# Optimization experiments

Measured on AMD Instinct MI355X. Metric: run time of the kernel, lower is better.

The kernel has to match this reference:

```python
import jax, jax.numpy as jnp
import numpy as np

B, N, V, H, R, A, IN, K = 64, 512, 64, 512, 4, 18, 128, 32
EPS = 1e-8


def setup_inputs() -> dict:
    key = jax.random.key(0)
    ks = jax.random.split(key, 20)
    g = lambda i, shape, s=1.0: jax.random.normal(ks[i], shape, jnp.float32) * s
    u = lambda i, shape: jax.random.uniform(ks[i], shape, dtype=jnp.float32)
    cin = IN + R * V
    return dict(
        x=g(0, (B, IN)),
        h=g(1, (B, H), 0.1),
        c=g(2, (B, H), 0.1),
        memory=g(3, (B, N, V), 0.1),
        read_weights=u(4, (B, R, N)),
        write_weights=u(5, (B, N)),
        usage=u(6, (B, N)),
        link_matrix=u(7, (B, N, N)) * 0.01,
        precedence_weights=u(8, (B, N)),
        W_ih=g(9, (4 * H, cin), 0.05), W_hh=g(10, (4 * H, H), 0.05),
        b_ih=jnp.zeros(4 * H, jnp.float32), b_hh=jnp.zeros(4 * H, jnp.float32),
        W_read=g(11, (R, V + 4, H), 0.05), b_read=jnp.zeros((R, V + 4), jnp.float32),
        W_write=g(12, (3 * V + 3, H), 0.05), b_write=jnp.zeros(3 * V + 3, jnp.float32),
        W_pol=g(13, (A, H), 0.05), b_pol=jnp.zeros(A, jnp.float32),
        W_val=g(14, (1, H), 0.05), b_val=jnp.zeros(1, jnp.float32),
    )


def reference(x, h, c, memory, read_weights, write_weights, usage, link_matrix,
              precedence_weights, W_ih, W_hh, b_ih, b_hh, W_read, b_read,
              W_write, b_write, W_pol, b_pol, W_val, b_val):
    # ---- read heads (vectorized over R) ----
    ro = jnp.einsum('roh,bh->bro', W_read, h) + b_read            # [B,R,V+4]
    rkey = ro[..., :V]
    rbeta = jax.nn.softplus(ro[..., V])                           # [B,R]
    rpi = jax.nn.softmax(ro[..., V + 1:V + 4], axis=-1)           # backward/content/forward gates
    mem_norm = jnp.maximum(jnp.linalg.norm(memory, axis=-1), EPS)  # [B,N]
    key_norm = jnp.maximum(jnp.linalg.norm(rkey, axis=-1), EPS)    # [B,R]
    sim = jnp.einsum('bnv,brv->brn', memory, rkey) / (mem_norm[:, None, :] * key_norm[..., None])
    scores = rbeta[..., None] * sim                                # [B,R,N]
    kth = jax.lax.top_k(scores, K)[0][..., -1:]                    # sparse top-k mask
    cw = jax.nn.softmax(jnp.where(scores >= kth, scores, -jnp.inf), axis=-1)
    fw = jnp.einsum('bnm,brm->brn', link_matrix, read_weights)     # forward weighting L w
    bw = jnp.einsum('bmn,brm->brn', link_matrix, read_weights)     # backward weighting L^T w
    w_r = rpi[..., 0:1] * bw + rpi[..., 1:2] * cw + rpi[..., 2:3] * fw  # [B,R,N]
    rvec = jnp.einsum('brn,bnv->brv', w_r, memory).reshape(B, R * V)
    # ---- LSTM controller (torch LSTMCell gate order i,f,g,o) ----
    gates = jnp.concatenate([x, rvec], -1) @ W_ih.T + h @ W_hh.T + b_ih + b_hh
    i_g, f_g, g_g, o_g = jnp.split(gates, 4, axis=-1)
    c_new = jax.nn.sigmoid(f_g) * c + jax.nn.sigmoid(i_g) * jnp.tanh(g_g)
    h_new = jax.nn.sigmoid(o_g) * jnp.tanh(c_new)
    # ---- write head ----
    wo = h_new @ W_write.T + b_write                               # [B,3V+3]
    wkey = wo[:, :V]
    erase = jax.nn.sigmoid(wo[:, V:2 * V])
    add = jnp.tanh(wo[:, 2 * V:3 * V])
    wbeta = jax.nn.softplus(wo[:, 3 * V])
    g_a = jax.nn.sigmoid(wo[:, 3 * V + 1])
    g_w = jax.nn.sigmoid(wo[:, 3 * V + 2])
    wkey_norm = jnp.maximum(jnp.linalg.norm(wkey, axis=-1), EPS)
    wsim = jnp.einsum('bnv,bv->bn', memory, wkey) / (mem_norm * wkey_norm[:, None])
    cw_w = jax.nn.softmax(wbeta[:, None] * wsim, axis=-1)
    # allocation weighting from sorted usage (DNC Eq. 1)
    idx = jnp.argsort(usage, axis=-1)
    u_sorted = jnp.take_along_axis(usage, idx, -1)
    prod_prev = jnp.concatenate([jnp.ones((B, 1), usage.dtype), jnp.cumprod(u_sorted, -1)[:, :-1]], -1)
    a_sorted = (1.0 - u_sorted) * prod_prev
    alloc = jnp.take_along_axis(a_sorted, jnp.argsort(idx, -1), -1)
    write_w = g_w[:, None] * (g_a[:, None] * alloc + (1.0 - g_a)[:, None] * cw_w)  # [B,N]
    # ---- memory erase/add ----
    mem_new = memory * (1.0 - write_w[:, :, None] * erase[:, None, :]) + write_w[:, :, None] * add[:, None, :]
    # ---- usage (psi detached as in torch.no_grad) ----
    psi = jax.lax.stop_gradient(jnp.prod(1.0 - w_r, axis=1))
    usage_new = (usage + write_weights - usage * write_weights) * psi
    # ---- link matrix + precedence ----
    ws = jnp.sum(write_w, -1, keepdims=True)
    prec_new = (1.0 - ws) * precedence_weights + write_w
    decay = (1.0 - write_w[:, :, None]) * (1.0 - write_w[:, None, :])
    link_new = decay * link_matrix + write_w[:, :, None] * precedence_weights[:, None, :]
    link_new = link_new * (1.0 - jnp.eye(N, dtype=link_new.dtype))
    # ---- actor/critic heads ----
    logits = h_new @ W_pol.T + b_pol
    value = h_new @ W_val.T + b_val
    return (logits, value, h_new, c_new, mem_new, w_r, write_w, usage_new, link_new, prec_new)
```

## Files before the change

### kernel.cpp

```cpp
#include <hip/hip_runtime.h>
#include <math.h>

constexpr int Bb = 64, Nn = 512, Vv = 64, Hh = 512, Rr = 4, Aa = 18, INp = 128, KTOP = 32;
constexpr int CIN = 384;
constexpr int WOUT = 195;
#define EPSf 1e-8f

__device__ __forceinline__ float sigmoidf(float x){ return 1.f/(1.f+expf(-x)); }
__device__ __forceinline__ float softplusf(float x){ return (x>20.f)? x : log1pf(expf(x)); }
__device__ __forceinline__ float wave_reduce(float v){
  #pragma unroll
  for(int o=32;o>0;o>>=1) v += __shfl_down(v, o, 64);
  return v;
}

__global__ void k_read_proj(const float* __restrict__ Wr, const float* __restrict__ br,
                            const float* __restrict__ h, float* __restrict__ ro) {
  int bid = blockIdx.x;
  int b = bid / 68;
  int p = (bid % 68) * 4 + (threadIdx.x >> 6);
  int lane = threadIdx.x & 63;
  const float* wrow = Wr + p * Hh;
  const float* hb = h + b * Hh;
  float acc = 0.f;
  #pragma unroll
  for (int t = 0; t < 8; ++t) { int k = lane + 64*t; acc += wrow[k] * hb[k]; }
  acc = wave_reduce(acc);
  if (lane == 0) ro[b*272 + p] = acc + br[p];
}

__global__ void k_scores(const float* __restrict__ mem, const float* __restrict__ ro,
                         float* __restrict__ scores) {
  int row = blockIdx.x*4 + (threadIdx.x>>6);
  int lane = threadIdx.x & 63;
  int b = row >> 9, n = row & 511;
  float m = mem[row*Vv + lane];
  float mn = wave_reduce(m*m);
  #pragma unroll
  for (int r = 0; r < Rr; ++r) {
    const float* rob = ro + b*272 + r*68;
    float kv = rob[lane];
    float s  = wave_reduce(m*kv);
    float k2 = wave_reduce(kv*kv);
    if (lane == 0) {
      float rbeta = softplusf(rob[64]);
      float mnc = fmaxf(sqrtf(mn), EPSf);
      float knc = fmaxf(sqrtf(k2), EPSf);
      scores[(b*Rr + r)*Nn + n] = rbeta * s / (mnc * knc);
    }
  }
}

__global__ void k_topk_cw(const float* __restrict__ scores, float* __restrict__ cw) {
  __shared__ float sv[512];
  __shared__ float so[512];
  __shared__ float red[256];
  int br = blockIdx.x;
  int tid = threadIdx.x;
  const float* srow = scores + br*Nn;
  for (int i = tid; i < 512; i += 256) { float v = srow[i]; sv[i]=v; so[i]=v; }
  __syncthreads();
  for (int k = 2; k <= 512; k <<= 1) {
    for (int j = k>>1; j > 0; j >>= 1) {
      for (int i = tid; i < 512; i += 256) {
        int ixj = i ^ j;
        if (ixj > i) {
          float a = sv[i], c = sv[ixj];
          bool descSeg = ((i & k) == 0);
          bool sw = descSeg ? (a < c) : (a > c);
          if (sw) { sv[i]=c; sv[ixj]=a; }
        }
      }
      __syncthreads();
    }
  }
  float kth = sv[KTOP-1];
  float mx = sv[0];
  float lsum = 0.f;
  for (int i = tid; i < 512; i += 256) {
    float v = so[i];
    lsum += (v >= kth) ? expf(v - mx) : 0.f;
  }
  red[tid] = lsum; __syncthreads();
  for (int s2 = 128; s2 > 0; s2 >>= 1) {
    if (tid < s2) red[tid] += red[tid+s2];
    __syncthreads();
  }
  float inv = 1.f / red[0];
  for (int i = tid; i < 512; i += 256) {
    float v = so[i];
    cw[br*Nn + i] = (v >= kth) ? expf(v - mx)*inv : 0.f;
  }
}

__global__ void k_fwbw(const float* __restrict__ link, const float* __restrict__ rw,
                       float* __restrict__ fw, float* __restrict__ bwpart) {
  __shared__ float bl[4][4][512];
  int b  = blockIdx.x >> 3;
  int ch = blockIdx.x & 7;
  int wv = threadIdx.x >> 6, lane = threadIdx.x & 63;
  const float* rwb = rw + b*Rr*Nn;
  float rwv[4][8];
  #pragma unroll
  for (int r = 0; r < 4; ++r)
    #pragma unroll
    for (int t = 0; t < 8; ++t) rwv[r][t] = rwb[r*512 + lane + 64*t];
  float bwacc[8][4] = {};
  const float* lb = link + (size_t)b*Nn*Nn;
  int n0 = ch*64 + wv*16;
  for (int i = 0; i < 16; ++i) {
    int n = n0 + i;
    float lk[8];
    #pragma unroll
    for (int t = 0; t < 8; ++t) lk[t] = lb[n*512 + lane + 64*t];
    float s0 = rwb[n], s1 = rwb[512+n], s2 = rwb[1024+n], s3 = rwb[1536+n];
    float f0=0,f1=0,f2=0,f3=0;
    #pragma unroll
    for (int t = 0; t < 8; ++t) {
      float lv = lk[t];
      f0 += lv*rwv[0][t]; f1 += lv*rwv[1][t]; f2 += lv*rwv[2][t]; f3 += lv*rwv[3][t];
      bwacc[t][0] += lv*s0; bwacc[t][1] += lv*s1; bwacc[t][2] += lv*s2; bwacc[t][3] += lv*s3;
    }
    f0 = wave_reduce(f0); f1 = wave_reduce(f1);
    f2 = wave_reduce(f2); f3 = wave_reduce(f3);
    if (lane == 0) {
      fw[(b*Rr+0)*Nn+n] = f0; fw[(b*Rr+1)*Nn+n] = f1;
      fw[(b*Rr+2)*Nn+n] = f2; fw[(b*Rr+3)*Nn+n] = f3;
    }
  }
  #pragma unroll
  for (int t = 0; t < 8; ++t)
    #pragma unroll
    for (int r = 0; r < 4; ++r) bl[wv][r][lane + 64*t] = bwacc[t][r];
  __syncthreads();
  int tid = threadIdx.x;
  #pragma unroll
  for (int q = 0; q < 8; ++q) {
    int idx = q*256 + tid;
    int r = idx >> 9, j = idx & 511;
    float v = bl[0][r][j] + bl[1][r][j] + bl[2][r][j] + bl[3][r][j];
    bwpart[((size_t)(ch*Bb + b)*Rr + r)*Nn + j] = v;
  }
}

__global__ void k_wr_usage(const float* __restrict__ bwpart, const float* __restrict__ cw,
                           const float* __restrict__ fw, const float* __restrict__ ro,
                           const float* __restrict__ usage, const float* __restrict__ wwt,
                           float* __restrict__ out_wr, float* __restrict__ out_usage,
                           float* __restrict__ ws_rvec) {
  int idx = blockIdx.x*256 + threadIdx.x;
  if (idx < Bb*Rr*Vv) ws_rvec[idx] = 0.f;
  int b = idx >> 9, n = idx & 511;
  float psi = 1.f;
  #pragma unroll
  for (int r = 0; r < Rr; ++r) {
    int br = b*Rr + r;
    const float* rob = ro + b*272 + r*68;
    float e0 = rob[65], e1 = rob[66], e2 = rob[67];
    float m = fmaxf(e0, fmaxf(e1, e2));
    float x0 = expf(e0-m), x1 = expf(e1-m), x2 = expf(e2-m);
    float inv = 1.f/(x0+x1+x2);
    float bwv = 0.f;
    #pragma unroll
    for (int chh = 0; chh < 8; ++chh)
      bwv += bwpart[((size_t)(chh*Bb + b)*Rr + r)*Nn + n];
    float w = (x0*bwv + x1*cw[br*Nn+n] + x2*fw[br*Nn+n]) * inv;
    out_wr[br*Nn+n] = w;
    psi *= (1.f - w);
  }
  float u = usage[idx], wt = wwt[idx];
  out_usage[idx] = (u + wt - u*wt) * psi;
}

__global__ void k_rvec(const float* __restrict__ wr, const float* __restrict__ mem,
                       float* __restrict__ rvec) {
  int b = blockIdx.x >> 3;
  int ch = blockIdx.x & 7;
  int r = threadIdx.x >> 6, v = threadIdx.x & 63;
  const float* wrow = wr + (b*Rr + r)*Nn;
  const float* mb = mem + (size_t)b*Nn*Vv;
  float acc = 0.f;
  #pragma unroll 4
  for (int t = 0; t < 64; ++t) {
    int n = ch*64 + t;
    acc += wrow[n] * mb[n*Vv + v];
  }
  atomicAdd(&rvec[(b*Rr+r)*Vv + v], acc);
}

__global__ void k_gates(const float* __restrict__ x, const float* __restrict__ rvec,
                        const float* __restrict__ h, const float* __restrict__ Wih,
                        const float* __restrict__ Whh, const float* __restrict__ bih,
                        const float* __restrict__ bhh, float* __restrict__ gates) {
  int gid = blockIdx.x*4 + (threadIdx.x>>6);
  int lane = threadIdx.x & 63;
  int jt = gid >> 4;
  int bt = gid & 15;
  float acc[4][4] = {};
  #pragma unroll
  for (int t = 0; t < 6; ++t) {
    int k = lane + 64*t;
    float u[4], w[4];
    #pragma unroll
    for (int i = 0; i < 4; ++i) {
      int b = bt*4 + i;
      u[i] = (k < INp) ? x[b*INp + k] : rvec[b*(Rr*Vv) + k - INp];
      w[i] = Wih[(jt*4+i)*CIN + k];
    }
    #pragma unroll
    for (int jj = 0; jj < 4; ++jj)
      #pragma unroll
      for (int bb = 0; bb < 4; ++bb) acc[jj][bb] += w[jj]*u[bb];
  }
  #pragma unroll
  for (int t = 0; t < 8; ++t) {
    int k = lane + 64*t;
    float u[4], w[4];
    #pragma unroll
    for (int i = 0; i < 4; ++i) {
      u[i] = h[(bt*4+i)*Hh + k];
      w[i] = Whh[(jt*4+i)*Hh + k];
    }
    #pragma unroll
    for (int jj = 0; jj < 4; ++jj)
      #pragma unroll
      for (int bb = 0; bb < 4; ++bb) acc[jj][bb] += w[jj]*u[bb];
  }
  #pragma unroll
  for (int jj = 0; jj < 4; ++jj)
    #pragma unroll
    for (int bb = 0; bb < 4; ++bb) {
      float v = wave_reduce(acc[jj][bb]);
      if (lane == 0) {
        int j = jt*4 + jj, b = bt*4 + bb;
        gates[b*(4*Hh) + j] = v + bih[j] + bhh[j];
      }
    }
}

__global__ void k_lstm(const float* __restrict__ gates, const float* __restrict__ c,
                       float* __restrict__ out_h, float* __restrict__ out_c) {
  int idx = blockIdx.x*256 + threadIdx.x;
  int b = idx >> 9, hh = idx & 511;
  const float* g = gates + b*2048;
  float ig = sigmoidf(g[hh]), fg = sigmoidf(g[512+hh]);
  float gg = tanhf(g[1024+hh]), og = sigmoidf(g[1536+hh]);
  float cn = fg * c[idx] + ig * gg;
  float hn = og * tanhf(cn);
  out_c[idx] = cn; out_h[idx] = hn;
}

__global__ void k_wopol(const float* __restrict__ hn, const float* __restrict__ Ww,
                        const float* __restrict__ bw_, const float* __restrict__ Wp,
                        const float* __restrict__ bp, const float* __restrict__ Wv,
                        const float* __restrict__ bv, float* __restrict__ wo,
                        float* __restrict__ out_logits, float* __restrict__ out_value) {
  int gid = blockIdx.x*4 + (threadIdx.x>>6);
  int lane = threadIdx.x & 63;
  int b = gid / 214, o = gid % 214;
  const float* wrow;
  if (o < WOUT) wrow = Ww + o*Hh;
  else if (o < WOUT + Aa) wrow = Wp + (o-WOUT)*Hh;
  else wrow = Wv;
  const float* hb = hn + b*Hh;
  float acc = 0.f;
  #pragma unroll
  for (int t = 0; t < 8; ++t) { int k = lane+64*t; acc += hb[k]*wrow[k]; }
  acc = wave_reduce(acc);
  if (lane == 0) {
    if (o < WOUT) wo[b*WOUT+o] = acc + bw_[o];
    else if (o < WOUT + Aa) out_logits[b*Aa + (o-WOUT)] = acc + bp[o-WOUT];
    else out_value[b] = acc + bv[0];
  }
}

__global__ void k_wsim(const float* __restrict__ mem, const float* __restrict__ wo,
                       float* __restrict__ wsim) {
  int row = blockIdx.x*4 + (threadIdx.x>>6);
  int lane = threadIdx.x & 63;
  int b = row >> 9;
  const float* wob = wo + b*WOUT;
  float kv = wob[lane];
  float m = mem[row*Vv + lane];
  float s  = wave_reduce(m*kv);
  float mn = wave_reduce(m*m);
  float k2 = wave_reduce(kv*kv);
  if (lane == 0) {
    float wbeta = softplusf(wob[192]);
    wsim[row] = wbeta * s / (fmaxf(sqrtf(mn),EPSf) * fmaxf(sqrtf(k2),EPSf));
  }
}

__global__ void k_alloc(const float* __restrict__ usage, const float* __restrict__ wo,
                        const float* __restrict__ wsim, const float* __restrict__ prec,
                        float* __restrict__ out_ww, float* __restrict__ out_prec) {
  __shared__ float uv[512];
  __shared__ int   ui[512];
  __shared__ float cp[512];
  __shared__ float al[512];
  __shared__ float red[256];
  int b = blockIdx.x, tid = threadIdx.x;
  float s0 = wsim[b*Nn + tid], s1 = wsim[b*Nn + tid + 256];
  red[tid] = fmaxf(s0, s1); __syncthreads();
  for (int s2=128; s2>0; s2>>=1){ if (tid<s2) red[tid]=fmaxf(red[tid],red[tid+s2]); __syncthreads(); }
  float mx = red[0]; __syncthreads();
  float e0 = expf(s0-mx), e1 = expf(s1-mx);
  red[tid] = e0+e1; __syncthreads();
  for (int s2=128; s2>0; s2>>=1){ if (tid<s2) red[tid]+=red[tid+s2]; __syncthreads(); }
  float cinv = 1.f/red[0];
  float c0 = e0*cinv, c1 = e1*cinv;
  __syncthreads();
  for (int i = tid; i < 512; i += 256) { uv[i] = usage[b*Nn+i]; ui[i] = i; }
  __syncthreads();
  for (int k = 2; k <= 512; k <<= 1) {
    for (int j = k>>1; j > 0; j >>= 1) {
      for (int i = tid; i < 512; i += 256) {
        int ixj = i ^ j;
        if (ixj > i) {
          float av = uv[i], bv = uv[ixj];
          int ai = ui[i], bi = ui[ixj];
          bool gt = (av > bv) || (av == bv && ai > bi);
          bool asc = ((i & k) == 0);
          bool sw = asc ? gt : !gt;
          if (sw) { uv[i]=bv; uv[ixj]=av; ui[i]=bi; ui[ixj]=ai; }
        }
      }
      __syncthreads();
    }
  }
  for (int i = tid; i < 512; i += 256) cp[i] = uv[i];
  __syncthreads();
  for (int d = 1; d < 512; d <<= 1) {
    float t0 = cp[tid]     * ((tid >= d)     ? cp[tid-d]     : 1.f);
    float t1 = cp[tid+256] * ((tid+256 >= d) ? cp[tid+256-d] : 1.f);
    __syncthreads();
    cp[tid] = t0; cp[tid+256] = t1;
    __syncthreads();
  }
  for (int i = tid; i < 512; i += 256) {
    float pp = (i == 0) ? 1.f : cp[i-1];
    al[ui[i]] = (1.f - uv[i]) * pp;
  }
  __syncthreads();
  float ga = sigmoidf(wo[b*WOUT+193]);
  float gw = sigmoidf(wo[b*WOUT+194]);
  int n0 = tid, n1 = tid+256;
  float wv0 = gw * (ga*al[n0] + (1.f-ga)*c0);
  float wv1 = gw * (ga*al[n1] + (1.f-ga)*c1);
  out_ww[b*Nn+n0] = wv0; out_ww[b*Nn+n1] = wv1;
  red[tid] = wv0 + wv1; __syncthreads();
  for (int s2=128; s2>0; s2>>=1){ if (tid<s2) red[tid]+=red[tid+s2]; __syncthreads(); }
  float wsum = red[0];
  out_prec[b*Nn+n0] = (1.f - wsum)*prec[b*Nn+n0] + wv0;
  out_prec[b*Nn+n1] = (1.f - wsum)*prec[b*Nn+n1] + wv1;
}

__global__ void k_memlink(const float* __restrict__ link, const float* __restrict__ ww,
                          const float* __restrict__ prec, const float* __restrict__ mem,
                          const float* __restrict__ wo, float* __restrict__ out_link,
                          float* __restrict__ out_mem) {
  int bid = blockIdx.x;
  if (bid < 16384) {
    int idx4 = bid*256 + threadIdx.x;
    int base = idx4*4;
    int b = base >> 18;
    int rem = base & 262143;
    int i = rem >> 9;
    int j0 = rem & 511;
    float wi = ww[b*Nn + i];
    float fi = 1.f - wi;
    float4 lv = *(const float4*)(link + base);
    float4 wj = *(const float4*)(ww + b*Nn + j0);
    float4 pj = *(const float4*)(prec + b*Nn + j0);
    float4 o;
    o.x = fi*(1.f-wj.x)*lv.x + wi*pj.x;
    o.y = fi*(1.f-wj.y)*lv.y + wi*pj.y;
    o.z = fi*(1.f-wj.z)*lv.z + wi*pj.z;
    o.w = fi*(1.f-wj.w)*lv.w + wi*pj.w;
    if (i >= j0 && i < j0+4) {
      if (i == j0) o.x = 0.f;
      else if (i == j0+1) o.y = 0.f;
      else if (i == j0+2) o.z = 0.f;
      else o.w = 0.f;
    }
    *(float4*)(out_link + base) = o;
  } else {
    int idx4 = (bid - 16384)*256 + threadIdx.x;
    int base = idx4*4;
    int b = base >> 15;
    int rem = base & 32767;
    int n = rem >> 6;
    int v0 = rem & 63;
    float w = ww[b*Nn + n];
    const float* wob = wo + b*WOUT;
    float4 m = *(const float4*)(mem + base);
    float4 o;
    float e, a;
    e = sigmoidf(wob[64+v0+0]); a = tanhf(wob[128+v0+0]); o.x = m.x*(1.f-w*e)+w*a;
    e = sigmoidf(wob[64+v0+1]); a = tanhf(wob[128+v0+1]); o.y = m.y*(1.f-w*e)+w*a;
    e = sigmoidf(wob[64+v0+2]); a = tanhf(wob[128+v0+2]); o.z = m.z*(1.f-w*e)+w*a;
    e = sigmoidf(wob[64+v0+3]); a = tanhf(wob[128+v0+3]); o.w = m.w*(1.f-w*e)+w*a;
    *(float4*)(out_mem + base) = o;
  }
}

extern "C" void kernel_launch(void* const* d_in, const int* in_sizes, int n_in,
                              void* d_out, int out_size, void* d_ws, size_t ws_size,
                              hipStream_t stream) {
  const float* x    = (const float*)d_in[0];
  const float* h    = (const float*)d_in[1];
  const float* c    = (const float*)d_in[2];
  const float* mem  = (const float*)d_in[3];
  const float* rw   = (const float*)d_in[4];
  const float* wwt  = (const float*)d_in[5];
  const float* usage= (const float*)d_in[6];
  const float* link = (const float*)d_in[7];
  const float* prec = (const float*)d_in[8];
  const float* Wih  = (const float*)d_in[9];
  const float* Whh  = (const float*)d_in[10];
  const float* bih  = (const float*)d_in[11];
  const float* bhh  = (const float*)d_in[12];
  const float* Wr   = (const float*)d_in[13];
  const float* br   = (const float*)d_in[14];
  const float* Ww   = (const float*)d_in[15];
  const float* bw_  = (const float*)d_in[16];
  const float* Wp   = (const float*)d_in[17];
  const float* bp   = (const float*)d_in[18];
  const float* Wv   = (const float*)d_in[19];
  const float* bv   = (const float*)d_in[20];

  float* out = (float*)d_out;
  float* o_logits = out + 0;
  float* o_value  = out + 1152;
  float* o_h      = out + 1216;
  float* o_c      = out + 33984;
  float* o_mem    = out + 66752;
  float* o_wr     = out + 2163904;
  float* o_ww     = out + 2294976;
  float* o_usage  = out + 2327744;
  float* o_link   = out + 2360512;
  float* o_prec   = out + 19137728;

  float* ws = (float*)d_ws;
  float* ws_ro     = ws;
  float* ws_sc     = ws + 17408;
  float* ws_cw     = ws + 148480;
  float* ws_fw     = ws + 279552;
  float* ws_bwpart = ws + 410624;
  float* ws_rvec   = ws + 1459200;
  float* ws_gates  = ws + 1475584;
  float* ws_wo     = ws + 1606656;
  float* ws_wsim   = ws + 1619136;

  k_read_proj <<<dim3(Bb*68),        dim3(256), 0, stream>>>(Wr, br, h, ws_ro);
  k_scores    <<<dim3(Bb*Nn/4),      dim3(256), 0, stream>>>(mem, ws_ro, ws_sc);
  k_topk_cw   <<<dim3(Bb*Rr),        dim3(256), 0, stream>>>(ws_sc, ws_cw);
  k_fwbw      <<<dim3(Bb*8),         dim3(256), 0, stream>>>(link, rw, ws_fw, ws_bwpart);
  k_wr_usage  <<<dim3(Bb*Nn/256),    dim3(256), 0, stream>>>(ws_bwpart, ws_cw, ws_fw, ws_ro, usage, wwt, o_wr, o_usage, ws_rvec);
  k_rvec      <<<dim3(Bb*8),         dim3(256), 0, stream>>>(o_wr, mem, ws_rvec);
  k_gates     <<<dim3(2048),         dim3(256), 0, stream>>>(x, ws_rvec, h, Wih, Whh, bih, bhh, ws_gates);
  k_lstm      <<<dim3(Bb*Hh/256),    dim3(256), 0, stream>>>(ws_gates, c, o_h, o_c);
  k_wopol     <<<dim3(Bb*214/4),     dim3(256), 0, stream>>>(o_h, Ww, bw_, Wp, bp, Wv, bv, ws_wo, o_logits, o_value);
  k_wsim      <<<dim3(Bb*Nn/4),      dim3(256), 0, stream>>>(mem, ws_wo, ws_wsim);
  k_alloc     <<<dim3(Bb),           dim3(256), 0, stream>>>(usage, ws_wo, ws_wsim, prec, o_ww, o_prec);
  k_memlink   <<<dim3(16384+2048),   dim3(256), 0, stream>>>(link, o_ww, prec, mem, ws_wo, o_link, o_mem);
}
```

Before: 347.6 us.

## Fuse kernels, replace bitonic sorts with rank counting, precompute read-head params

Merges the read projection with the forward/backward link pass in one launch, folds the read-vector product into the read-weight kernel, and fuses the LSTM gate GEMV with the cell update. The bitonic sorts in top-k and allocation become O(N^2) rank counting on packed order keys. Softmax gates, key norms and inverse memory norms are computed once and reused. Launch count, sync barriers and intermediate traffic drop. The cost is fewer blocks in the read-vector kernel (128) and serial 512-step rank loops per thread.

```diff
diff --git a/kernel.cpp b/kernel.cpp
--- a/kernel.cpp
+++ b/kernel.cpp
@@ -13,188 +13,209 @@
   for(int o=32;o>0;o>>=1) v += __shfl_down(v, o, 64);
   return v;
 }
-
-__global__ void k_read_proj(const float* __restrict__ Wr, const float* __restrict__ br,
-                            const float* __restrict__ h, float* __restrict__ ro) {
-  int bid = blockIdx.x;
-  int b = bid / 68;
-  int p = (bid % 68) * 4 + (threadIdx.x >> 6);
-  int lane = threadIdx.x & 63;
-  const float* wrow = Wr + p * Hh;
-  const float* hb = h + b * Hh;
-  float acc = 0.f;
-  #pragma unroll
-  for (int t = 0; t < 8; ++t) { int k = lane + 64*t; acc += wrow[k] * hb[k]; }
-  acc = wave_reduce(acc);
-  if (lane == 0) ro[b*272 + p] = acc + br[p];
+__device__ __forceinline__ unsigned f2ord(float f){
+  unsigned u = __float_as_uint(f);
+  return (u & 0x80000000u) ? ~u : (u | 0x80000000u);
+}
+
+__global__ void k_stage1(const float* __restrict__ link, const float* __restrict__ rw,
+                         const float* __restrict__ Wr, const float* __restrict__ brd,
+                         const float* __restrict__ h,
+                         float* __restrict__ fw, float* __restrict__ bwpart,
+                         float* __restrict__ rvec,
+                         float* __restrict__ ro, float* __restrict__ rp) {
+  __shared__ float bl[4][4][512];
+  __shared__ float sh[512];
+  __shared__ float sro[68];
+  if (blockIdx.x < 512) {
+    if (blockIdx.x < 64) rvec[blockIdx.x*256 + threadIdx.x] = 0.f;
+    int b  = blockIdx.x >> 3;
+    int ch = blockIdx.x & 7;
+    int wv = threadIdx.x >> 6, lane = threadIdx.x & 63;
+    const float* rwb = rw + b*Rr*Nn;
+    float rwv[4][8];
+    #pragma unroll
+    for (int r = 0; r < 4; ++r)
+      #pragma unroll
+      for (int t = 0; t < 8; ++t) rwv[r][t] = rwb[r*512 + lane + 64*t];
+    float bwacc[8][4] = {};
+    const float* lb = link + (size_t)b*Nn*Nn;
+    int n0 = ch*64 + wv*16;
+    for (int i = 0; i < 16; ++i) {
+      int n = n0 + i;
+      float lk[8];
+      #pragma unroll
+      for (int t = 0; t < 8; ++t) lk[t] = lb[n*512 + lane + 64*t];
+      float s0 = rwb[n], s1 = rwb[512+n], s2 = rwb[1024+n], s3 = rwb[1536+n];
+      float f0=0,f1=0,f2=0,f3=0;
+      #pragma unroll
+      for (int t = 0; t < 8; ++t) {
+        float lv = lk[t];
+        f0 += lv*rwv[0][t]; f1 += lv*rwv[1][t]; f2 += lv*rwv[2][t]; f3 += lv*rwv[3][t];
+        bwacc[t][0] += lv*s0; bwacc[t][1] += lv*s1; bwacc[t][2] += lv*s2; bwacc[t][3] += lv*s3;
+      }
+      f0 = wave_reduce(f0); f1 = wave_reduce(f1);
+      f2 = wave_reduce(f2); f3 = wave_reduce(f3);
+      if (lane == 0) {
+        fw[(b*Rr+0)*Nn+n] = f0; fw[(b*Rr+1)*Nn+n] = f1;
+        fw[(b*Rr+2)*Nn+n] = f2; fw[(b*Rr+3)*Nn+n] = f3;
+      }
+    }
+    #pragma unroll
+    for (int t = 0; t < 8; ++t)
+      #pragma unroll
+      for (int r = 0; r < 4; ++r) bl[wv][r][lane + 64*t] = bwacc[t][r];
+    __syncthreads();
+    int tid = threadIdx.x;
+    #pragma unroll
+    for (int q = 0; q < 8; ++q) {
+      int idx = q*256 + tid;
+      int r = idx >> 9, j = idx & 511;
+      float v = bl[0][r][j] + bl[1][r][j] + bl[2][r][j] + bl[3][r][j];
+      bwpart[((size_t)(ch*Bb + b)*Rr + r)*Nn + j] = v;
+    }
+  } else {
+    int blk = blockIdx.x - 512;
+    int b = blk >> 2, r = blk & 3;
+    int wv = threadIdx.x >> 6, lane = threadIdx.x & 63;
+    const float* hb = h + b*Hh;
+    for (int i = threadIdx.x; i < 512; i += 256) sh[i] = hb[i];
+    __syncthreads();
+    const float* wbase = Wr + (size_t)(r*68)*Hh;
+    for (int q = 0; q < 17; ++q) {
+      int p = wv*17 + q;
+      const float* wrow = wbase + (size_t)p*Hh;
+      float acc = 0.f;
+      #pragma unroll
+      for (int t = 0; t < 8; ++t) { int k = lane + 64*t; acc += wrow[k]*sh[k]; }
+      acc = wave_reduce(acc);
+      if (lane == 0) sro[p] = acc + brd[r*68 + p];
+    }
+    __syncthreads();
+    if (threadIdx.x < 68) ro[b*272 + r*68 + threadIdx.x] = sro[threadIdx.x];
+    if (wv == 0) {
+      float kv = sro[lane];
+      float k2 = wave_reduce(kv*kv);
+      if (lane == 0) {
+        float rbeta = softplusf(sro[64]);
+        float sc = rbeta / fmaxf(sqrtf(k2), EPSf);
+        float e0 = sro[65], e1 = sro[66], e2 = sro[67];
+        float mm = fmaxf(e0, fmaxf(e1, e2));
+        float x0 = expf(e0-mm), x1 = expf(e1-mm), x2 = expf(e2-mm);
+        float inv = 1.f/(x0+x1+x2);
+        float* rpb = rp + (b*4 + r)*4;
+        rpb[0] = sc; rpb[1] = x0*inv; rpb[2] = x1*inv; rpb[3] = x2*inv;
+      }
+    }
+  }
 }
 
 __global__ void k_scores(const float* __restrict__ mem, const float* __restrict__ ro,
-                         float* __restrict__ scores) {
+                         const float* __restrict__ rp, float* __restrict__ scores,
+                         float* __restrict__ invmn) {
   int row = blockIdx.x*4 + (threadIdx.x>>6);
   int lane = threadIdx.x & 63;
   int b = row >> 9, n = row & 511;
   float m = mem[row*Vv + lane];
-  float mn = wave_reduce(m*m);
-  #pragma unroll
-  for (int r = 0; r < Rr; ++r) {
-    const float* rob = ro + b*272 + r*68;
-    float kv = rob[lane];
-    float s  = wave_reduce(m*kv);
-    float k2 = wave_reduce(kv*kv);
-    if (lane == 0) {
-      float rbeta = softplusf(rob[64]);
-      float mnc = fmaxf(sqrtf(mn), EPSf);
-      float knc = fmaxf(sqrtf(k2), EPSf);
-      scores[(b*Rr + r)*Nn + n] = rbeta * s / (mnc * knc);
-    }
+  const float* rob = ro + b*272;
+  float v0 = m*m;
+  float v1 = m * rob[lane];
+  float v2 = m * rob[68  + lane];
+  float v3 = m * rob[136 + lane];
+  float v4 = m * rob[204 + lane];
+  #pragma unroll
+  for (int o = 32; o > 0; o >>= 1) {
+    v0 += __shfl_down(v0,o,64); v1 += __shfl_down(v1,o,64);
+    v2 += __shfl_down(v2,o,64); v3 += __shfl_down(v3,o,64);
+    v4 += __shfl_down(v4,o,64);
+  }
+  if (lane == 0) {
+    float im = 1.f / fmaxf(sqrtf(v0), EPSf);
+    invmn[row] = im;
+    const float* rpb = rp + b*16;
+    scores[(b*4+0)*Nn+n] = rpb[0]  * v1 * im;
+    scores[(b*4+1)*Nn+n] = rpb[4]  * v2 * im;
+    scores[(b*4+2)*Nn+n] = rpb[8]  * v3 * im;
+    scores[(b*4+3)*Nn+n] = rpb[12] * v4 * im;
   }
 }
 
 __global__ void k_topk_cw(const float* __restrict__ scores, float* __restrict__ cw) {
-  __shared__ float sv[512];
-  __shared__ float so[512];
-  __shared__ float red[256];
-  int br = blockIdx.x;
+  __shared__ unsigned long long sk[512];
+  __shared__ float sred[4];
+  __shared__ float skv[2];
+  int br = blockIdx.x, tid = threadIdx.x;
+  float v0 = scores[br*Nn + tid], v1 = scores[br*Nn + tid + 256];
+  unsigned long long k0 = ((unsigned long long)f2ord(v0) << 32) | (unsigned)(511 - tid);
+  unsigned long long k1 = ((unsigned long long)f2ord(v1) << 32) | (unsigned)(255 - tid);
+  sk[tid] = k0; sk[tid+256] = k1;
+  __syncthreads();
+  int c0 = 0, c1 = 0;
+  #pragma unroll 8
+  for (int j = 0; j < 512; ++j) {
+    unsigned long long kj = sk[j];
+    c0 += (kj > k0); c1 += (kj > k1);
+  }
+  if (c0 == KTOP-1) skv[0] = v0;
+  if (c1 == KTOP-1) skv[0] = v1;
+  if (c0 == 0) skv[1] = v0;
+  if (c1 == 0) skv[1] = v1;
+  __syncthreads();
+  float kth = skv[0], mx = skv[1];
+  float e0 = (v0 >= kth) ? expf(v0-mx) : 0.f;
+  float e1 = (v1 >= kth) ? expf(v1-mx) : 0.f;
+  float s = wave_reduce(e0+e1);
+  if ((tid&63) == 0) sred[tid>>6] = s;
+  __syncthreads();
+  float inv = 1.f/(sred[0]+sred[1]+sred[2]+sred[3]);
+  cw[br*Nn+tid]     = e0*inv;
+  cw[br*Nn+tid+256] = e1*inv;
+}
+
+__global__ void k_wrrv(const float* __restrict__ bwpart, const float* __restrict__ cw,
+                       const float* __restrict__ fw, const float* __restrict__ rp,
+                       const float* __restrict__ usage, const float* __restrict__ wwt,
+                       const float* __restrict__ mem,
+                       float* __restrict__ out_wr, float* __restrict__ out_usage,
+                       float* __restrict__ rvec) {
+  __shared__ float swr[4][256];
+  int b = blockIdx.x >> 1, ch = blockIdx.x & 1;
   int tid = threadIdx.x;
-  const float* srow = scores + br*Nn;
-  for (int i = tid; i < 512; i += 256) { float v = srow[i]; sv[i]=v; so[i]=v; }
-  __syncthreads();
-  for (int k = 2; k <= 512; k <<= 1) {
-    for (int j = k>>1; j > 0; j >>= 1) {
-      for (int i = tid; i < 512; i += 256) {
-        int ixj = i ^ j;
-        if (ixj > i) {
-          float a = sv[i], c = sv[ixj];
-          bool descSeg = ((i & k) == 0);
-          bool sw = descSeg ? (a < c) : (a > c);
-          if (sw) { sv[i]=c; sv[ixj]=a; }
-        }
-      }
-      __syncthreads();
-    }
-  }
-  float kth = sv[KTOP-1];
-  float mx = sv[0];
-  float lsum = 0.f;
-  for (int i = tid; i < 512; i += 256) {
-    float v = so[i];
-    lsum += (v >= kth) ? expf(v - mx) : 0.f;
-  }
-  red[tid] = lsum; __syncthreads();
-  for (int s2 = 128; s2 > 0; s2 >>= 1) {
-    if (tid < s2) red[tid] += red[tid+s2];
-    __syncthreads();
-  }
-  float inv = 1.f / red[0];
-  for (int i = tid; i < 512; i += 256) {
-    float v = so[i];
-    cw[br*Nn + i] = (v >= kth) ? expf(v - mx)*inv : 0.f;
-  }
-}
-
-__global__ void k_fwbw(const float* __restrict__ link, const float* __restrict__ rw,
-                       float* __restrict__ fw, float* __restrict__ bwpart) {
-  __shared__ float bl[4][4][512];
-  int b  = blockIdx.x >> 3;
-  int ch = blockIdx.x & 7;
-  int wv = threadIdx.x >> 6, lane = threadIdx.x & 63;
-  const float* rwb = rw + b*Rr*Nn;
-  float rwv[4][8];
-  #pragma unroll
-  for (int r = 0; r < 4; ++r)
-    #pragma unroll
-    for (int t = 0; t < 8; ++t) rwv[r][t] = rwb[r*512 + lane + 64*t];
-  float bwacc[8][4] = {};
-  const float* lb = link + (size_t)b*Nn*Nn;
-  int n0 = ch*64 + wv*16;
-  for (int i = 0; i < 16; ++i) {
-    int n = n0 + i;
-    float lk[8];
-    #pragma unroll
-    for (int t = 0; t < 8; ++t) lk[t] = lb[n*512 + lane + 64*t];
-    float s0 = rwb[n], s1 = rwb[512+n], s2 = rwb[1024+n], s3 = rwb[1536+n];
-    float f0=0,f1=0,f2=0,f3=0;
-    #pragma unroll
-    for (int t = 0; t < 8; ++t) {
-      float lv = lk[t];
-      f0 += lv*rwv[0][t]; f1 += lv*rwv[1][t]; f2 += lv*rwv[2][t]; f3 += lv*rwv[3][t];
-      bwacc[t][0] += lv*s0; bwacc[t][1] += lv*s1; bwacc[t][2] += lv*s2; bwacc[t][3] += lv*s3;
-    }
-    f0 = wave_reduce(f0); f1 = wave_reduce(f1);
-    f2 = wave_reduce(f2); f3 = wave_reduce(f3);
-    if (lane == 0) {
-      fw[(b*Rr+0)*Nn+n] = f0; fw[(b*Rr+1)*Nn+n] = f1;
-      fw[(b*Rr+2)*Nn+n] = f2; fw[(b*Rr+3)*Nn+n] = f3;
-    }
-  }
-  #pragma unroll
-  for (int t = 0; t < 8; ++t)
-    #pragma unroll
-    for (int r = 0; r < 4; ++r) bl[wv][r][lane + 64*t] = bwacc[t][r];
-  __syncthreads();
-  int tid = threadIdx.x;
-  #pragma unroll
-  for (int q = 0; q < 8; ++q) {
-    int idx = q*256 + tid;
-    int r = idx >> 9, j = idx & 511;
-    float v = bl[0][r][j] + bl[1][r][j] + bl[2][r][j] + bl[3][r][j];
-    bwpart[((size_t)(ch*Bb + b)*Rr + r)*Nn + j] = v;
-  }
-}
-
-__global__ void k_wr_usage(const float* __restrict__ bwpart, const float* __restrict__ cw,
-                           const float* __restrict__ fw, const float* __restrict__ ro,
-                           const float* __restrict__ usage, const float* __restrict__ wwt,
-                           float* __restrict__ out_wr, float* __restrict__ out_usage,
-                           float* __restrict__ ws_rvec) {
-  int idx = blockIdx.x*256 + threadIdx.x;
-  if (idx < Bb*Rr*Vv) ws_rvec[idx] = 0.f;
-  int b = idx >> 9, n = idx & 511;
+  int n = ch*256 + tid;
+  int idx = b*Nn + n;
   float psi = 1.f;
   #pragma unroll
-  for (int r = 0; r < Rr; ++r) {
-    int br = b*Rr + r;
-    const float* rob = ro + b*272 + r*68;
-    float e0 = rob[65], e1 = rob[66], e2 = rob[67];
-    float m = fmaxf(e0, fmaxf(e1, e2));
-    float x0 = expf(e0-m), x1 = expf(e1-m), x2 = expf(e2-m);
-    float inv = 1.f/(x0+x1+x2);
+  for (int r = 0; r < 4; ++r) {
+    int brr = b*4 + r;
     float bwv = 0.f;
     #pragma unroll
     for (int chh = 0; chh < 8; ++chh)
       bwv += bwpart[((size_t)(chh*Bb + b)*Rr + r)*Nn + n];
-    float w = (x0*bwv + x1*cw[br*Nn+n] + x2*fw[br*Nn+n]) * inv;
-    out_wr[br*Nn+n] = w;
+    const float* rpb = rp + brr*4;
+    float w = rpb[1]*bwv + rpb[2]*cw[brr*Nn+n] + rpb[3]*fw[brr*Nn+n];
+    out_wr[brr*Nn+n] = w;
+    swr[r][tid] = w;
     psi *= (1.f - w);
   }
   float u = usage[idx], wt = wwt[idx];
   out_usage[idx] = (u + wt - u*wt) * psi;
-}
-
-__global__ void k_rvec(const float* __restrict__ wr, const float* __restrict__ mem,
-                       float* __restrict__ rvec) {
-  int b = blockIdx.x >> 3;
-  int ch = blockIdx.x & 7;
-  int r = threadIdx.x >> 6, v = threadIdx.x & 63;
-  const float* wrow = wr + (b*Rr + r)*Nn;
-  const float* mb = mem + (size_t)b*Nn*Vv;
+  __syncthreads();
+  int r = tid >> 6, v = tid & 63;
+  const float* mb = mem + ((size_t)b*Nn + ch*256)*Vv + v;
   float acc = 0.f;
   #pragma unroll 4
-  for (int t = 0; t < 64; ++t) {
-    int n = ch*64 + t;
-    acc += wrow[n] * mb[n*Vv + v];
-  }
-  atomicAdd(&rvec[(b*Rr+r)*Vv + v], acc);
-}
-
-__global__ void k_gates(const float* __restrict__ x, const float* __restrict__ rvec,
-                        const float* __restrict__ h, const float* __restrict__ Wih,
-                        const float* __restrict__ Whh, const float* __restrict__ bih,
-                        const float* __restrict__ bhh, float* __restrict__ gates) {
+  for (int t = 0; t < 256; ++t) acc += swr[r][t] * mb[t*Vv];
+  atomicAdd(&rvec[(b*4+r)*Vv + v], acc);
+}
+
+__global__ void k_gates_lstm(const float* __restrict__ x, const float* __restrict__ rvec,
+                             const float* __restrict__ h, const float* __restrict__ Wih,
+                             const float* __restrict__ Whh, const float* __restrict__ bih,
+                             const float* __restrict__ bhh, const float* __restrict__ c,
+                             float* __restrict__ out_h, float* __restrict__ out_c) {
   int gid = blockIdx.x*4 + (threadIdx.x>>6);
   int lane = threadIdx.x & 63;
-  int jt = gid >> 4;
+  int hh = gid >> 4;
   int bt = gid & 15;
   float acc[4][4] = {};
   #pragma unroll
@@ -205,12 +226,12 @@
     for (int i = 0; i < 4; ++i) {
       int b = bt*4 + i;
       u[i] = (k < INp) ? x[b*INp + k] : rvec[b*(Rr*Vv) + k - INp];
-      w[i] = Wih[(jt*4+i)*CIN + k];
-    }
-    #pragma unroll
-    for (int jj = 0; jj < 4; ++jj)
-      #pragma unroll
-      for (int bb = 0; bb < 4; ++bb) acc[jj][bb] += w[jj]*u[bb];
+      w[i] = Wih[(size_t)(i*Hh + hh)*CIN + k];
+    }
+    #pragma unroll
+    for (int g = 0; g < 4; ++g)
+      #pragma unroll
+      for (int bb = 0; bb < 4; ++bb) acc[g][bb] += w[g]*u[bb];
   }
   #pragma unroll
   for (int t = 0; t < 8; ++t) {
@@ -219,35 +240,34 @@
     #pragma unroll
     for (int i = 0; i < 4; ++i) {
       u[i] = h[(bt*4+i)*Hh + k];
-      w[i] = Whh[(jt*4+i)*Hh + k];
-    }
-    #pragma unroll
-    for (int jj = 0; jj < 4; ++jj)
-      #pragma unroll
-      for (int bb = 0; bb < 4; ++bb) acc[jj][bb] += w[jj]*u[bb];
-  }
-  #pragma unroll
-  for (int jj = 0; jj < 4; ++jj)
+      w[i] = Whh[(size_t)(i*Hh + hh)*Hh + k];
+    }
+    #pragma unroll
+    for (int g = 0; g < 4; ++g)
+      #pragma unroll
+      for (int bb = 0; bb < 4; ++bb) acc[g][bb] += w[g]*u[bb];
+  }
+  #pragma unroll
+  for (int g = 0; g < 4; ++g)
+    #pragma unroll
+    for (int bb = 0; bb < 4; ++bb) acc[g][bb] = wave_reduce(acc[g][bb]);
+  if (lane == 0) {
+    float bsum[4];
+    #pragma unroll
+    for (int g = 0; g < 4; ++g) bsum[g] = bih[g*Hh + hh] + bhh[g*Hh + hh];
     #pragma unroll
     for (int bb = 0; bb < 4; ++bb) {
-      float v = wave_reduce(acc[jj][bb]);
-      if (lane == 0) {
-        int j = jt*4 + jj, b = bt*4 + bb;
-        gates[b*(4*Hh) + j] = v + bih[j] + bhh[j];
-      }
-    }
-}
-
-__global__ void k_lstm(const float* __restrict__ gates, const float* __restrict__ c,
-                       float* __restrict__ out_h, float* __restrict__ out_c) {
-  int idx = blockIdx.x*256 + threadIdx.x;
-  int b = idx >> 9, hh = idx & 511;
-  const float* g = gates + b*2048;
-  float ig = sigmoidf(g[hh]), fg = sigmoidf(g[512+hh]);
-  float gg = tanhf(g[1024+hh]), og = sigmoidf(g[1536+hh]);
-  float cn = fg * c[idx] + ig * gg;
-  float hn = og * tanhf(cn);
-  out_c[idx] = cn; out_h[idx] = hn;
+      int b = bt*4 + bb;
+      float ig = sigmoidf(acc[0][bb] + bsum[0]);
+      float fg = sigmoidf(acc[1][bb] + bsum[1]);
+      float gg = tanhf   (acc[2][bb] + bsum[2]);
+      float og = sigmoidf(acc[3][bb] + bsum[3]);
+      float cn = fg * c[b*Hh + hh] + ig * gg;
+      float hn = og * tanhf(cn);
+      out_c[b*Hh + hh] = cn;
+      out_h[b*Hh + hh] = hn;
+    }
+  }
 }
 
 __global__ void k_wopol(const float* __restrict__ hn, const float* __restrict__ Ww,
@@ -275,60 +295,59 @@
 }
 
 __global__ void k_wsim(const float* __restrict__ mem, const float* __restrict__ wo,
-                       float* __restrict__ wsim) {
+                       const float* __restrict__ invmn, float* __restrict__ wsim) {
   int row = blockIdx.x*4 + (threadIdx.x>>6);
   int lane = threadIdx.x & 63;
   int b = row >> 9;
   const float* wob = wo + b*WOUT;
   float kv = wob[lane];
   float m = mem[row*Vv + lane];
-  float s  = wave_reduce(m*kv);
-  float mn = wave_reduce(m*m);
-  float k2 = wave_reduce(kv*kv);
+  float v0 = m*kv, v1 = kv*kv;
+  #pragma unroll
+  for (int o = 32; o > 0; o >>= 1) {
+    v0 += __shfl_down(v0,o,64); v1 += __shfl_down(v1,o,64);
+  }
   if (lane == 0) {
     float wbeta = softplusf(wob[192]);
-    wsim[row] = wbeta * s / (fmaxf(sqrtf(mn),EPSf) * fmaxf(sqrtf(k2),EPSf));
+    wsim[row] = wbeta * v0 * invmn[row] / fmaxf(sqrtf(v1), EPSf);
   }
 }
 
 __global__ void k_alloc(const float* __restrict__ usage, const float* __restrict__ wo,
                         const float* __restrict__ wsim, const float* __restrict__ prec,
                         float* __restrict__ out_ww, float* __restrict__ out_prec) {
-  __shared__ float uv[512];
-  __shared__ int   ui[512];
+  __shared__ unsigned long long sk[512];
+  __shared__ float su[512];
   __shared__ float cp[512];
-  __shared__ float al[512];
-  __shared__ float red[256];
+  __shared__ float sred[8];
   int b = blockIdx.x, tid = threadIdx.x;
-  float s0 = wsim[b*Nn + tid], s1 = wsim[b*Nn + tid + 256];
-  red[tid] = fmaxf(s0, s1); __syncthreads();
-  for (int s2=128; s2>0; s2>>=1){ if (tid<s2) red[tid]=fmaxf(red[tid],red[tid+s2]); __syncthreads(); }
-  float mx = red[0]; __syncthreads();
+  int wv = tid >> 6, lane = tid & 63;
+  float s0 = wsim[b*Nn+tid], s1 = wsim[b*Nn+tid+256];
+  float u0 = usage[b*Nn+tid], u1 = usage[b*Nn+tid+256];
+  unsigned long long k0 = ((unsigned long long)f2ord(u0) << 32) | (unsigned)tid;
+  unsigned long long k1 = ((unsigned long long)f2ord(u1) << 32) | (unsigned)(tid+256);
+  sk[tid] = k0; sk[tid+256] = k1;
+  float mxl = fmaxf(s0, s1);
+  #pragma unroll
+  for (int o = 32; o > 0; o >>= 1) mxl = fmaxf(mxl, __shfl_down(mxl,o,64));
+  if (lane == 0) sred[wv] = mxl;
+  __syncthreads();
+  float mx = fmaxf(fmaxf(sred[0],sred[1]), fmaxf(sred[2],sred[3]));
   float e0 = expf(s0-mx), e1 = expf(s1-mx);
-  red[tid] = e0+e1; __syncthreads();
-  for (int s2=128; s2>0; s2>>=1){ if (tid<s2) red[tid]+=red[tid+s2]; __syncthreads(); }
-  float cinv = 1.f/red[0];
+  float ssum = wave_reduce(e0+e1);
+  if (lane == 0) sred[4+wv] = ssum;
+  int r0 = 0, r1 = 0;
+  #pragma unroll 8
+  for (int j = 0; j < 512; ++j) {
+    unsigned long long kj = sk[j];
+    r0 += (kj < k0); r1 += (kj < k1);
+  }
+  __syncthreads();
+  float cinv = 1.f/(sred[4]+sred[5]+sred[6]+sred[7]);
   float c0 = e0*cinv, c1 = e1*cinv;
-  __syncthreads();
-  for (int i = tid; i < 512; i += 256) { uv[i] = usage[b*Nn+i]; ui[i] = i; }
-  __syncthreads();
-  for (int k = 2; k <= 512; k <<= 1) {
-    for (int j = k>>1; j > 0; j >>= 1) {
-      for (int i = tid; i < 512; i += 256) {
-        int ixj = i ^ j;
-        if (ixj > i) {
-          float av = uv[i], bv = uv[ixj];
-          int ai = ui[i], bi = ui[ixj];
-          bool gt = (av > bv) || (av == bv && ai > bi);
-          bool asc = ((i & k) == 0);
-          bool sw = asc ? gt : !gt;
-          if (sw) { uv[i]=bv; uv[ixj]=av; ui[i]=bi; ui[ixj]=ai; }
-        }
-      }
-      __syncthreads();
-    }
-  }
-  for (int i = tid; i < 512; i += 256) cp[i] = uv[i];
+  su[r0] = u0; su[r1] = u1;
+  __syncthreads();
+  cp[tid] = su[tid]; cp[tid+256] = su[tid+256];
   __syncthreads();
   for (int d = 1; d < 512; d <<= 1) {
     float t0 = cp[tid]     * ((tid >= d)     ? cp[tid-d]     : 1.f);
@@ -337,22 +356,21 @@
     cp[tid] = t0; cp[tid+256] = t1;
     __syncthreads();
   }
-  for (int i = tid; i < 512; i += 256) {
-    float pp = (i == 0) ? 1.f : cp[i-1];
-    al[ui[i]] = (1.f - uv[i]) * pp;
-  }
-  __syncthreads();
+  float pp0 = (r0 == 0) ? 1.f : cp[r0-1];
+  float pp1 = (r1 == 0) ? 1.f : cp[r1-1];
+  float a0 = (1.f-u0)*pp0, a1 = (1.f-u1)*pp1;
   float ga = sigmoidf(wo[b*WOUT+193]);
   float gw = sigmoidf(wo[b*WOUT+194]);
-  int n0 = tid, n1 = tid+256;
-  float wv0 = gw * (ga*al[n0] + (1.f-ga)*c0);
-  float wv1 = gw * (ga*al[n1] + (1.f-ga)*c1);
-  out_ww[b*Nn+n0] = wv0; out_ww[b*Nn+n1] = wv1;
-  red[tid] = wv0 + wv1; __syncthreads();
-  for (int s2=128; s2>0; s2>>=1){ if (tid<s2) red[tid]+=red[tid+s2]; __syncthreads(); }
-  float wsum = red[0];
-  out_prec[b*Nn+n0] = (1.f - wsum)*prec[b*Nn+n0] + wv0;
-  out_prec[b*Nn+n1] = (1.f - wsum)*prec[b*Nn+n1] + wv1;
+  float wv0 = gw * (ga*a0 + (1.f-ga)*c0);
+  float wv1 = gw * (ga*a1 + (1.f-ga)*c1);
+  out_ww[b*Nn+tid]     = wv0;
+  out_ww[b*Nn+tid+256] = wv1;
+  float ws_ = wave_reduce(wv0+wv1);
+  if (lane == 0) sred[wv] = ws_;
+  __syncthreads();
+  float wsum = sred[0]+sred[1]+sred[2]+sred[3];
+  out_prec[b*Nn+tid]     = (1.f-wsum)*prec[b*Nn+tid]     + wv0;
+  out_prec[b*Nn+tid+256] = (1.f-wsum)*prec[b*Nn+tid+256] + wv1;
 }
 
 __global__ void k_memlink(const float* __restrict__ link, const float* __restrict__ ww,
@@ -443,25 +461,23 @@
 
   float* ws = (float*)d_ws;
   float* ws_ro     = ws;
-  float* ws_sc     = ws + 17408;
-  float* ws_cw     = ws + 148480;
-  float* ws_fw     = ws + 279552;
-  float* ws_bwpart = ws + 410624;
-  float* ws_rvec   = ws + 1459200;
-  float* ws_gates  = ws + 1475584;
-  float* ws_wo     = ws + 1606656;
-  float* ws_wsim   = ws + 1619136;
-
-  k_read_proj <<<dim3(Bb*68),        dim3(256), 0, stream>>>(Wr, br, h, ws_ro);
-  k_scores    <<<dim3(Bb*Nn/4),      dim3(256), 0, stream>>>(mem, ws_ro, ws_sc);
-  k_topk_cw   <<<dim3(Bb*Rr),        dim3(256), 0, stream>>>(ws_sc, ws_cw);
-  k_fwbw      <<<dim3(Bb*8),         dim3(256), 0, stream>>>(link, rw, ws_fw, ws_bwpart);
-  k_wr_usage  <<<dim3(Bb*Nn/256),    dim3(256), 0, stream>>>(ws_bwpart, ws_cw, ws_fw, ws_ro, usage, wwt, o_wr, o_usage, ws_rvec);
-  k_rvec      <<<dim3(Bb*8),         dim3(256), 0, stream>>>(o_wr, mem, ws_rvec);
-  k_gates     <<<dim3(2048),         dim3(256), 0, stream>>>(x, ws_rvec, h, Wih, Whh, bih, bhh, ws_gates);
-  k_lstm      <<<dim3(Bb*Hh/256),    dim3(256), 0, stream>>>(ws_gates, c, o_h, o_c);
-  k_wopol     <<<dim3(Bb*214/4),     dim3(256), 0, stream>>>(o_h, Ww, bw_, Wp, bp, Wv, bv, ws_wo, o_logits, o_value);
-  k_wsim      <<<dim3(Bb*Nn/4),      dim3(256), 0, stream>>>(mem, ws_wo, ws_wsim);
-  k_alloc     <<<dim3(Bb),           dim3(256), 0, stream>>>(usage, ws_wo, ws_wsim, prec, o_ww, o_prec);
-  k_memlink   <<<dim3(16384+2048),   dim3(256), 0, stream>>>(link, o_ww, prec, mem, ws_wo, o_link, o_mem);
-}
+  float* ws_rp     = ws + 17408;
+  float* ws_sc     = ws + 18432;
+  float* ws_cw     = ws + 149504;
+  float* ws_fw     = ws + 280576;
+  float* ws_bwpart = ws + 411648;
+  float* ws_rvec   = ws + 1460224;
+  float* ws_wo     = ws + 1476608;
+  float* ws_wsim   = ws + 1489088;
+  float* ws_invmn  = ws + 1521856;
+
+  k_stage1     <<<dim3(768),       dim3(256), 0, stream>>>(link, rw, Wr, br, h, ws_fw, ws_bwpart, ws_rvec, ws_ro, ws_rp);
+  k_scores     <<<dim3(Bb*Nn/4),   dim3(256), 0, stream>>>(mem, ws_ro, ws_rp, ws_sc, ws_invmn);
+  k_topk_cw    <<<dim3(Bb*Rr),     dim3(256), 0, stream>>>(ws_sc, ws_cw);
+  k_wrrv       <<<dim3(Bb*2),      dim3(256), 0, stream>>>(ws_bwpart, ws_cw, ws_fw, ws_rp, usage, wwt, mem, o_wr, o_usage, ws_rvec);
+  k_gates_lstm <<<dim3(2048),      dim3(256), 0, stream>>>(x, ws_rvec, h, Wih, Whh, bih, bhh, c, o_h, o_c);
+  k_wopol      <<<dim3(Bb*214/4),  dim3(256), 0, stream>>>(o_h, Ww, bw_, Wp, bp, Wv, bv, ws_wo, o_logits, o_value);
+  k_wsim       <<<dim3(Bb*Nn/4),   dim3(256), 0, stream>>>(mem, ws_wo, ws_invmn, ws_wsim);
+  k_alloc      <<<dim3(Bb),        dim3(256), 0, stream>>>(usage, ws_wo, ws_wsim, prec, o_ww, o_prec);
+  k_memlink    <<<dim3(16384+2048),dim3(256), 0, stream>>>(link, o_ww, prec, mem, ws_wo, o_link, o_mem);
+}
```

Result: faster. 296.3 us (-14.8%).
